# Optimization experiments

Hardware: AMD Instinct MI355X
Metric: run time of the kernel (lower is better)

Reference implementation:

```python
import jax, jax.numpy as jnp
import numpy as np

# Module hyperparameters (init_kwargs)
NH = 254          # nHidden
NSTEP = 32        # MPC horizon
DT = 1.0 / 60.0   # del_t
EPS = 1e-4
PQ = 5.0
QV = 200.0
QA = 1.0
N_STATE = NH + 2  # hidden embedding + [position, velocity]
NBATCH = 256


def setup_inputs() -> dict:
    key = jax.random.key(0)
    k1, k2, k3, k4, k5, k6 = jax.random.split(key, 6)
    x = jax.random.normal(k1, (NBATCH, NH), dtype=jnp.float32)
    gripper_p = jax.random.normal(k2, (NBATCH,), dtype=jnp.float32)
    own_gripper_v = jax.random.normal(k3, (NBATCH,), dtype=jnp.float32)
    other_gripper_v = jax.random.normal(k4, (NBATCH,), dtype=jnp.float32)
    # Learned parameters (as in __init__): Af ~ U[0,1), Lq = tril(U[0,1))
    Af = jax.random.uniform(k5, (NH, 1), dtype=jnp.float32)
    Lq = jnp.tril(jax.random.uniform(k6, (NH, NH), dtype=jnp.float32))
    return {"x": x, "gripper_p": gripper_p, "own_gripper_v": own_gripper_v,
            "other_gripper_v": other_gripper_v, "Af": Af, "Lq": Lq}


def _mpc_forward(x, gripper_p, own_gripper_v, Af, Lq):
    n = N_STATE
    dt = x.dtype
    eye_n = jnp.eye(n, dtype=dt)

    # ---- Q0: [[Lq Lq^T + eps I, 0], [0, diag(0, Qv)]]  (n x n) ----
    Q0_tl = Lq @ Lq.T + EPS * jnp.eye(NH, dtype=dt)
    Q0 = jnp.zeros((n, n), dt).at[:NH, :NH].set(Q0_tl).at[NH + 1, NH + 1].set(QV)
    w = jnp.ones((NSTEP,), dt).at[-1].set(PQ)        # final-step weight Pq
    Q0_stack = w[:, None, None] * Q0                 # [NSTEP, n, n]
    Q_dia = jax.scipy.linalg.block_diag(*Q0_stack)   # [NSTEP*n, NSTEP*n]

    # ---- A0: [[I, 0, Af], [0, 1, dt], [0, 0, 1]] ----
    A0 = jnp.zeros((n, n), dt)
    A0 = A0.at[:NH, :NH].set(jnp.eye(NH, dtype=dt)).at[:NH, NH + 1].set(Af[:, 0])
    A0 = A0.at[NH, NH].set(1.0).at[NH, NH + 1].set(DT).at[NH + 1, NH + 1].set(1.0)

    # ---- powers A0^1..A0^NSTEP via scan (replaces the Python power loop) ----
    def step(carry, _):
        nxt = carry @ A0
        return nxt, nxt
    _, Pk = jax.lax.scan(step, eye_n, None, length=NSTEP)   # Pk[k] = A0^{k+1}
    P = jnp.concatenate([eye_n[None], Pk], axis=0)          # A0^0 .. A0^NSTEP
    T_ = Pk.reshape(NSTEP * n, n)                           # vstack(A0^1..A0^NSTEP)

    # ---- AN_: block lower-triangular Toeplitz, block (i,j) = A0^{i-j} for j<=i ----
    d = jnp.arange(NSTEP)[:, None] - jnp.arange(NSTEP)[None, :]
    blocks = jnp.where((d >= 0)[:, :, None, None],
                       P[jnp.clip(d, 0, NSTEP)], jnp.zeros((), dt))  # [NSTEP,NSTEP,n,n]
    AN_ = blocks.transpose(0, 2, 1, 3).reshape(NSTEP * n, NSTEP * n)

    B0 = jnp.zeros((n, 1), dt).at[NH, 0].set(0.5 * DT * DT).at[NH + 1, 0].set(DT)
    B_dia = jax.scipy.linalg.block_diag(*jnp.broadcast_to(B0, (NSTEP, n, 1)))

    S_ = AN_ @ B_dia                                        # [NSTEP*n, NSTEP]
    QS = Q_dia @ S_                                         # [NSTEP*n, NSTEP]
    Q_final = 2.0 * (QA * jnp.eye(NSTEP, dtype=dt) + S_.T @ QS) \
              + EPS * jnp.eye(NSTEP, dtype=dt)
    p_final = 2.0 * (T_.T @ QS)                             # [n, NSTEP]

    # ---- batch state x0 = [x, gripper_p, own_gripper_v] ----
    x0 = jnp.concatenate([x, gripper_p[:, None], own_gripper_v[:, None]], axis=1)
    p_x0 = x0 @ p_final                                     # [B, NSTEP]

    # QPFunction with G=0, h=0, no equalities -> unconstrained QP:
    # u = argmin 0.5 u^T Q_final u + p_x0^T u = -Q_final^{-1} p_x0
    u = -jnp.linalg.solve(Q_final, p_x0.T).T                # [B, NSTEP]

    # x_predict = S u + T x0 ; output picks position component (index NH) per step
    x_pred = u @ S_.T + x0 @ T_.T                           # [B, NSTEP*n]
    posi = x_pred.reshape(-1, NSTEP, n)[:, :, NH]           # [B, NSTEP]
    return posi


def reference(x, gripper_p, own_gripper_v, other_gripper_v, Af, Lq):
    # other_gripper_v is accepted but unused in the active forward path (as in source)
    return _mpc_forward(x, gripper_p, own_gripper_v, Af, Lq)
```

## Files before the change

kernel.cpp:

```cpp
#include <hip/hip_runtime.h>

#define NH 254
#define NSTEP 32
#define NB 256

constexpr float  FEPS = 1e-4f;
constexpr double DDT  = 1.0 / 60.0;
constexpr double DQV  = 200.0;
constexpr double DPQ  = 5.0;
constexpr double DQA  = 1.0;
constexpr double DEPS = 1e-4;

__global__ __launch_bounds__(256) void k_tg(const float* __restrict__ Lq,
                                            const float* __restrict__ Af,
                                            float* __restrict__ g,
                                            float* __restrict__ coef) {
    __shared__ float t_sh[256];
    __shared__ float af_sh[256];
    const int k    = threadIdx.x;
    const int lane = k & 63;
    const int w    = k >> 6;

    af_sh[k] = (k < NH) ? Af[k] : 0.f;
    __syncthreads();

    float acc = 0.f;
    if (k < NH) {
        #pragma unroll 8
        for (int i = 64 * w; i < NH; ++i)
            acc += Lq[i * NH + k] * af_sh[i];
    }
    t_sh[k] = acc;
    __syncthreads();

    if (blockIdx.x < 32) {
        const int i0 = blockIdx.x * 8;
        for (int rr = 0; rr < 2; ++rr) {
            const int i = i0 + 2 * w + rr;
            if (i >= NH) break;
            float a2 = 0.f;
            #pragma unroll
            for (int c4 = 0; c4 < 4; ++c4) {
                int kk = lane + 64 * c4;
                if (kk <= i) a2 += Lq[i * NH + kk] * t_sh[kk];
            }
            #pragma unroll
            for (int off = 32; off; off >>= 1) a2 += __shfl_xor(a2, off, 64);
            if (lane == 0) g[i] = a2 + FEPS * Af[i];
        }
        return;
    }

    __shared__ double red[4];
    __shared__ double M[32][34];
    __shared__ double ua[32], ub[32];

    double v = 0.0;
    if (k < NH) {
        double td = (double)t_sh[k];
        double ad = (double)af_sh[k];
        v = td * td + DEPS * ad * ad;
    }
    #pragma unroll
    for (int off = 32; off; off >>= 1) v += __shfl_xor(v, off, 64);
    if (lane == 0) red[w] = v;
    __syncthreads();
    const double c = red[0] + red[1] + red[2] + red[3];

    for (int e = k; e < 1024; e += 256) {
        const int j1 = e >> 5, j2 = e & 31;
        const int m = (j1 > j2) ? j1 : j2;
        double s = 0.0;
        for (int kk = m; kk < 32; ++kk) {
            const double wk = (kk == 31) ? DPQ : 1.0;
            s += wk * ((double)(kk - j1) * (double)(kk - j2) * c + DQV);
        }
        M[j1][j2] = 2.0 * DDT * DDT * s + ((j1 == j2) ? (2.0 * DQA + DEPS) : 0.0);
    }
    if (k < 32) {
        const int j = k;
        double sa = 0.0, sb = 0.0;
        for (int kk = j; kk < 32; ++kk) {
            const double wk = (kk == 31) ? DPQ : 1.0;
            sa += wk * (double)(kk - j);
            sb += wk * ((double)(kk + 1) * (double)(kk - j) * c + DQV);
        }
        M[j][32] = 2.0 * DDT * sa;
        M[j][33] = 2.0 * DDT * sb;
    }
    __syncthreads();

    const int r  = k & 31;
    const int cg = k >> 5;
    for (int p = 0; p < 32; ++p) {
        const double f = M[r][p] / M[p][p];
        if (r != p) {
            for (int cc = cg; cc < 34; cc += 8)
                if (cc > p) M[r][cc] -= f * M[p][cc];
        }
        __syncthreads();
    }

    if (k < 32) {
        ua[k] = -M[k][32] / M[k][k];
        ub[k] = -M[k][33] / M[k][k];
    }
    __syncthreads();

    if (k < 32) {
        const int i = k;
        double ca = 0.0, cb = 0.0;
        for (int j = 0; j <= i; ++j) {
            const double wgt = (double)(i - j) + 0.5;
            ca += wgt * ua[j];
            cb += wgt * ub[j];
        }
        ca *= DDT * DDT;
        cb *= DDT * DDT;
        coef[i]      = (float)ca;
        coef[32 + i] = (float)((double)(i + 1) * DDT + cb);
    }
}

__global__ __launch_bounds__(64) void k_out(const float* __restrict__ x,
                                            const float* __restrict__ gp,
                                            const float* __restrict__ gv,
                                            const float* __restrict__ g,
                                            const float* __restrict__ coef,
                                            float* __restrict__ out) {
    const int b = blockIdx.x;
    const int lane = threadIdx.x;
    float acc = 0.f;
    #pragma unroll
    for (int c4 = 0; c4 < 4; ++c4) {
        const int kk = lane + 64 * c4;
        if (kk < NH) acc += x[b * NH + kk] * g[kk];
    }
    #pragma unroll
    for (int off = 32; off; off >>= 1) acc += __shfl_xor(acc, off, 64);
    if (lane < 32) {
        out[b * NSTEP + lane] = gp[b] + gv[b] * coef[32 + lane] + acc * coef[lane];
    }
}

extern "C" void kernel_launch(void* const* d_in, const int* in_sizes, int n_in,
                              void* d_out, int out_size, void* d_ws, size_t ws_size,
                              hipStream_t stream) {
    const float* x  = (const float*)d_in[0];
    const float* gp = (const float*)d_in[1];
    const float* gv = (const float*)d_in[2];
    const float* Af = (const float*)d_in[4];
    const float* Lq = (const float*)d_in[5];
    float* out = (float*)d_out;

    float* ws   = (float*)d_ws;
    float* g    = ws;
    float* coef = ws + 256;

    k_tg<<<33, 256, 0, stream>>>(Lq, Af, g, coef);
    k_out<<<NB, 64, 0, stream>>>(x, gp, gv, g, coef, out);
}
```

Measured before the change: 99.59 us.

## Fuse both kernels into one cooperative kernel with grid-wide syncs

Merges the Lq/Af reduction, the QP coefficient solve and the batched output into a single cooperative launch of 65 blocks. Each of 64 blocks reads four rows of Lq once, writes partial Lq^T·Af sums, and after a grid sync reduces them and reuses its cached rows for the Lq·t product. The block-per-row serial loop of the old first kernel is replaced. This removes a kernel launch and the long sequential column loop, but adds two grid.sync barriers and a 64-way partial reduction through global memory.

```diff
diff --git a/kernel.cpp b/kernel.cpp
--- a/kernel.cpp
+++ b/kernel.cpp
@@ -1,8 +1,12 @@
 #include <hip/hip_runtime.h>
+#include <hip/hip_cooperative_groups.h>
+
+namespace cg = cooperative_groups;
 
 #define NH 254
 #define NSTEP 32
 #define NB 256
+#define NBLK 65
 
 constexpr float  FEPS = 1e-4f;
 constexpr double DDT  = 1.0 / 60.0;
@@ -11,135 +15,162 @@
 constexpr double DQA  = 1.0;
 constexpr double DEPS = 1e-4;
 
-__global__ __launch_bounds__(256) void k_tg(const float* __restrict__ Lq,
-                                            const float* __restrict__ Af,
-                                            float* __restrict__ g,
-                                            float* __restrict__ coef) {
-    __shared__ float t_sh[256];
-    __shared__ float af_sh[256];
+__global__ __launch_bounds__(256) void k_all(const float* __restrict__ Lq,
+                                             const float* __restrict__ Af,
+                                             const float* __restrict__ x,
+                                             const float* __restrict__ gp,
+                                             const float* __restrict__ gv,
+                                             float* __restrict__ ws,
+                                             float* __restrict__ out) {
+    float* partial = ws;
+    float* g       = ws + 64 * 256;
+    float* coef    = g + 256;
+
+    __shared__ float  lq_sh[4][256];
+    __shared__ float  sh[256];
+    __shared__ double red[4];
+    __shared__ double M[32][34];
+    __shared__ double ua[32], ub[32];
+
+    const int bid  = blockIdx.x;
     const int k    = threadIdx.x;
     const int lane = k & 63;
     const int w    = k >> 6;
 
-    af_sh[k] = (k < NH) ? Af[k] : 0.f;
-    __syncthreads();
+    cg::grid_group grid = cg::this_grid();
 
-    float acc = 0.f;
-    if (k < NH) {
-        #pragma unroll 8
-        for (int i = 64 * w; i < NH; ++i)
-            acc += Lq[i * NH + k] * af_sh[i];
+    float xr[4] = {0.f, 0.f, 0.f, 0.f};
+    float gpv = 0.f, gvv = 0.f;
+
+    if (bid < 64) {
+        float lqv[4];
+        #pragma unroll
+        for (int j = 0; j < 4; ++j) {
+            const int i = 4 * bid + j;
+            lqv[j] = (i < NH && k < NH) ? Lq[i * NH + k] : 0.f;
+        }
+        const int r = 4 * bid + w;
+        #pragma unroll
+        for (int c4 = 0; c4 < 4; ++c4) {
+            const int kk = lane + 64 * c4;
+            xr[c4] = (kk < NH) ? x[r * NH + kk] : 0.f;
+        }
+        gpv = gp[r];
+        gvv = gv[r];
+
+        float acc = 0.f;
+        #pragma unroll
+        for (int j = 0; j < 4; ++j) {
+            const int i = 4 * bid + j;
+            const float afv = (i < NH) ? Af[i] : 0.f;
+            lq_sh[j][k] = lqv[j];
+            acc += lqv[j] * afv;
+        }
+        partial[bid * 256 + k] = acc;
     }
-    t_sh[k] = acc;
-    __syncthreads();
+    grid.sync();
 
-    if (blockIdx.x < 32) {
-        const int i0 = blockIdx.x * 8;
-        for (int rr = 0; rr < 2; ++rr) {
-            const int i = i0 + 2 * w + rr;
-            if (i >= NH) break;
-            float a2 = 0.f;
-            #pragma unroll
-            for (int c4 = 0; c4 < 4; ++c4) {
-                int kk = lane + 64 * c4;
-                if (kk <= i) a2 += Lq[i * NH + kk] * t_sh[kk];
-            }
-            #pragma unroll
-            for (int off = 32; off; off >>= 1) a2 += __shfl_xor(a2, off, 64);
-            if (lane == 0) g[i] = a2 + FEPS * Af[i];
-        }
-        return;
-    }
-
-    __shared__ double red[4];
-    __shared__ double M[32][34];
-    __shared__ double ua[32], ub[32];
-
-    double v = 0.0;
-    if (k < NH) {
-        double td = (double)t_sh[k];
-        double ad = (double)af_sh[k];
-        v = td * td + DEPS * ad * ad;
-    }
-    #pragma unroll
-    for (int off = 32; off; off >>= 1) v += __shfl_xor(v, off, 64);
-    if (lane == 0) red[w] = v;
-    __syncthreads();
-    const double c = red[0] + red[1] + red[2] + red[3];
-
-    for (int e = k; e < 1024; e += 256) {
-        const int j1 = e >> 5, j2 = e & 31;
-        const int m = (j1 > j2) ? j1 : j2;
-        double s = 0.0;
-        for (int kk = m; kk < 32; ++kk) {
-            const double wk = (kk == 31) ? DPQ : 1.0;
-            s += wk * ((double)(kk - j1) * (double)(kk - j2) * c + DQV);
-        }
-        M[j1][j2] = 2.0 * DDT * DDT * s + ((j1 == j2) ? (2.0 * DQA + DEPS) : 0.0);
-    }
-    if (k < 32) {
-        const int j = k;
-        double sa = 0.0, sb = 0.0;
-        for (int kk = j; kk < 32; ++kk) {
-            const double wk = (kk == 31) ? DPQ : 1.0;
-            sa += wk * (double)(kk - j);
-            sb += wk * ((double)(kk + 1) * (double)(kk - j) * c + DQV);
-        }
-        M[j][32] = 2.0 * DDT * sa;
-        M[j][33] = 2.0 * DDT * sb;
+    {
+        float tk = 0.f;
+        #pragma unroll 16
+        for (int b = 0; b < 64; ++b) tk += partial[b * 256 + k];
+        sh[k] = tk;
     }
     __syncthreads();
 
-    const int r  = k & 31;
-    const int cg = k >> 5;
-    for (int p = 0; p < 32; ++p) {
-        const double f = M[r][p] / M[p][p];
-        if (r != p) {
-            for (int cc = cg; cc < 34; cc += 8)
-                if (cc > p) M[r][cc] -= f * M[p][cc];
+    if (bid < 64) {
+        const int i = 4 * bid + w;
+        float a2 = 0.f;
+        #pragma unroll
+        for (int c4 = 0; c4 < 4; ++c4) {
+            const int kk = lane + 64 * c4;
+            a2 += lq_sh[w][kk] * sh[kk];
+        }
+        #pragma unroll
+        for (int off = 32; off; off >>= 1) a2 += __shfl_xor(a2, off, 64);
+        if (lane == 0 && i < NH) g[i] = a2 + FEPS * Af[i];
+    } else {
+        double v = 0.0;
+        if (k < NH) {
+            const double td = (double)sh[k];
+            const double ad = (double)Af[k];
+            v = td * td + DEPS * ad * ad;
+        }
+        #pragma unroll
+        for (int off = 32; off; off >>= 1) v += __shfl_xor(v, off, 64);
+        if (lane == 0) red[w] = v;
+        __syncthreads();
+        const double c = red[0] + red[1] + red[2] + red[3];
+
+        for (int e = k; e < 1024; e += 256) {
+            const int j1 = e >> 5, j2 = e & 31;
+            const int m = (j1 > j2) ? j1 : j2;
+            double s = 0.0;
+            for (int kk = m; kk < 32; ++kk) {
+                const double wk = (kk == 31) ? DPQ : 1.0;
+                s += wk * ((double)(kk - j1) * (double)(kk - j2) * c + DQV);
+            }
+            M[j1][j2] = 2.0 * DDT * DDT * s + ((j1 == j2) ? (2.0 * DQA + DEPS) : 0.0);
+        }
+        if (k < 32) {
+            const int j = k;
+            double sa = 0.0, sb = 0.0;
+            for (int kk = j; kk < 32; ++kk) {
+                const double wk = (kk == 31) ? DPQ : 1.0;
+                sa += wk * (double)(kk - j);
+                sb += wk * ((double)(kk + 1) * (double)(kk - j) * c + DQV);
+            }
+            M[j][32] = 2.0 * DDT * sa;
+            M[j][33] = 2.0 * DDT * sb;
         }
         __syncthreads();
+
+        const int r   = k & 31;
+        const int cg8 = k >> 5;
+        for (int p = 0; p < 32; ++p) {
+            const double f = M[r][p] / M[p][p];
+            if (r != p) {
+                for (int cc = cg8; cc < 34; cc += 8)
+                    if (cc > p) M[r][cc] -= f * M[p][cc];
+            }
+            __syncthreads();
+        }
+
+        if (k < 32) {
+            ua[k] = -M[k][32] / M[k][k];
+            ub[k] = -M[k][33] / M[k][k];
+        }
+        __syncthreads();
+
+        if (k < 32) {
+            const int i = k;
+            double ca = 0.0, cb = 0.0;
+            for (int j = 0; j <= i; ++j) {
+                const double wgt = (double)(i - j) + 0.5;
+                ca += wgt * ua[j];
+                cb += wgt * ub[j];
+            }
+            ca *= DDT * DDT;
+            cb *= DDT * DDT;
+            coef[i]      = (float)ca;
+            coef[32 + i] = (float)((double)(i + 1) * DDT + cb);
+        }
     }
+    __threadfence();
+    grid.sync();
 
-    if (k < 32) {
-        ua[k] = -M[k][32] / M[k][k];
-        ub[k] = -M[k][33] / M[k][k];
-    }
-    __syncthreads();
-
-    if (k < 32) {
-        const int i = k;
-        double ca = 0.0, cb = 0.0;
-        for (int j = 0; j <= i; ++j) {
-            const double wgt = (double)(i - j) + 0.5;
-            ca += wgt * ua[j];
-            cb += wgt * ub[j];
-        }
-        ca *= DDT * DDT;
-        cb *= DDT * DDT;
-        coef[i]      = (float)ca;
-        coef[32 + i] = (float)((double)(i + 1) * DDT + cb);
-    }
-}
-
-__global__ __launch_bounds__(64) void k_out(const float* __restrict__ x,
-                                            const float* __restrict__ gp,
-                                            const float* __restrict__ gv,
-                                            const float* __restrict__ g,
-                                            const float* __restrict__ coef,
-                                            float* __restrict__ out) {
-    const int b = blockIdx.x;
-    const int lane = threadIdx.x;
-    float acc = 0.f;
-    #pragma unroll
-    for (int c4 = 0; c4 < 4; ++c4) {
-        const int kk = lane + 64 * c4;
-        if (kk < NH) acc += x[b * NH + kk] * g[kk];
-    }
-    #pragma unroll
-    for (int off = 32; off; off >>= 1) acc += __shfl_xor(acc, off, 64);
-    if (lane < 32) {
-        out[b * NSTEP + lane] = gp[b] + gv[b] * coef[32 + lane] + acc * coef[lane];
+    if (bid < 64) {
+        sh[k] = (k < NH) ? g[k] : 0.f;
+        __syncthreads();
+        float s = 0.f;
+        #pragma unroll
+        for (int c4 = 0; c4 < 4; ++c4)
+            s += xr[c4] * sh[lane + 64 * c4];
+        #pragma unroll
+        for (int off = 32; off; off >>= 1) s += __shfl_xor(s, off, 64);
+        const int r = 4 * bid + w;
+        if (lane < 32)
+            out[r * NSTEP + lane] = gpv + gvv * coef[32 + lane] + s * coef[lane];
     }
 }
 
@@ -152,11 +183,10 @@
     const float* Af = (const float*)d_in[4];
     const float* Lq = (const float*)d_in[5];
     float* out = (float*)d_out;
+    float* ws  = (float*)d_ws;
 
-    float* ws   = (float*)d_ws;
-    float* g    = ws;
-    float* coef = ws + 256;
-
-    k_tg<<<33, 256, 0, stream>>>(Lq, Af, g, coef);
-    k_out<<<NB, 64, 0, stream>>>(x, gp, gv, g, coef, out);
+    void* args[] = {(void*)&Lq, (void*)&Af, (void*)&x, (void*)&gp, (void*)&gv,
+                    (void*)&ws, (void*)&out};
+    hipLaunchCooperativeKernel((const void*)k_all, dim3(NBLK), dim3(256),
+                               args, 0, stream);
 }
```

Result: slower. 125.1 us (+25.6%).

## Fuse both kernels into a single 1024-thread monolithic block

Applied to the files above, without the earlier changes.

Replaces the two-kernel pipeline (33-block setup kernel plus 256-block output kernel) with one 1024-thread single-block kernel. Lq·Af is split across four thread quarters, g = Lq t is kept in shared memory, and the 32x32 Gauss-Jordan solve plus the batch outputs are all computed in the same block. This removes one launch and the global round trip for g and coef, and drops the redundant per-block recomputation of t. In exchange, all Lq and x traffic now goes through a single CU, with far less memory parallelism.

```diff
diff --git a/kernel.cpp b/kernel.cpp
--- a/kernel.cpp
+++ b/kernel.cpp
@@ -11,64 +11,98 @@
 constexpr double DQA  = 1.0;
 constexpr double DEPS = 1e-4;
 
-__global__ __launch_bounds__(256) void k_tg(const float* __restrict__ Lq,
-                                            const float* __restrict__ Af,
-                                            float* __restrict__ g,
-                                            float* __restrict__ coef) {
-    __shared__ float t_sh[256];
-    __shared__ float af_sh[256];
-    const int k    = threadIdx.x;
-    const int lane = k & 63;
-    const int w    = k >> 6;
-
-    af_sh[k] = (k < NH) ? Af[k] : 0.f;
-    __syncthreads();
-
-    float acc = 0.f;
-    if (k < NH) {
-        #pragma unroll 8
-        for (int i = 64 * w; i < NH; ++i)
-            acc += Lq[i * NH + k] * af_sh[i];
-    }
-    t_sh[k] = acc;
-    __syncthreads();
-
-    if (blockIdx.x < 32) {
-        const int i0 = blockIdx.x * 8;
-        for (int rr = 0; rr < 2; ++rr) {
-            const int i = i0 + 2 * w + rr;
-            if (i >= NH) break;
-            float a2 = 0.f;
-            #pragma unroll
-            for (int c4 = 0; c4 < 4; ++c4) {
-                int kk = lane + 64 * c4;
-                if (kk <= i) a2 += Lq[i * NH + kk] * t_sh[kk];
-            }
-            #pragma unroll
-            for (int off = 32; off; off >>= 1) a2 += __shfl_xor(a2, off, 64);
-            if (lane == 0) g[i] = a2 + FEPS * Af[i];
-        }
-        return;
-    }
-
+__global__ __launch_bounds__(1024) void k_mono(const float* __restrict__ Lq,
+                                               const float* __restrict__ Af,
+                                               const float* __restrict__ x,
+                                               const float* __restrict__ gp,
+                                               const float* __restrict__ gv,
+                                               float* __restrict__ out) {
+    __shared__ float  af_sh[256];
+    __shared__ float  tpart[4][256];
+    __shared__ float  t_sh[256];
+    __shared__ float  g_sh[256];
     __shared__ double red[4];
     __shared__ double M[32][34];
     __shared__ double ua[32], ub[32];
+    __shared__ float  cA[32], cB[32];
 
-    double v = 0.0;
-    if (k < NH) {
-        double td = (double)t_sh[k];
-        double ad = (double)af_sh[k];
-        v = td * td + DEPS * ad * ad;
+    const int tid  = threadIdx.x;
+    const int k8   = tid & 255;
+    const int q    = tid >> 8;
+    const int lane = tid & 63;
+    const int wv   = tid >> 6;
+
+    if (q == 0) af_sh[k8] = (k8 < NH) ? Af[k8] : 0.f;
+    if (tid == 0) { g_sh[254] = 0.f; g_sh[255] = 0.f; }
+    __syncthreads();
+
+    {
+        float acc = 0.f;
+        const int ibase = q * 64;
+        if (k8 < NH && k8 < ibase + 64) {
+            const int iend = (ibase + 64 < NH) ? ibase + 64 : NH;
+            for (int i0 = ibase; i0 < iend; i0 += 8) {
+                float v[8];
+                #pragma unroll
+                for (int j = 0; j < 8; ++j)
+                    v[j] = (i0 + j < iend) ? Lq[(i0 + j) * NH + k8] : 0.f;
+                #pragma unroll
+                for (int j = 0; j < 8; ++j)
+                    acc += v[j] * af_sh[i0 + j];
+            }
+        }
+        tpart[q][k8] = acc;
     }
-    #pragma unroll
-    for (int off = 32; off; off >>= 1) v += __shfl_xor(v, off, 64);
-    if (lane == 0) red[w] = v;
+    __syncthreads();
+    if (tid < 256)
+        t_sh[tid] = tpart[0][tid] + tpart[1][tid] + tpart[2][tid] + tpart[3][tid];
+    __syncthreads();
+
+    for (int r = 0; r < 16; r += 2) {
+        const int i1 = wv + 16 * r;
+        const int i2 = i1 + 16;
+        float lv1[4], lv2[4];
+        #pragma unroll
+        for (int c = 0; c < 4; ++c) {
+            const int kk = lane + 64 * c;
+            lv1[c] = (kk <= i1) ? Lq[i1 * NH + kk] : 0.f;
+            lv2[c] = (i2 < NH && kk <= i2) ? Lq[i2 * NH + kk] : 0.f;
+        }
+        float a1 = 0.f, a2 = 0.f;
+        #pragma unroll
+        for (int c = 0; c < 4; ++c) {
+            const int kk = lane + 64 * c;
+            a1 += lv1[c] * t_sh[kk];
+            a2 += lv2[c] * t_sh[kk];
+        }
+        #pragma unroll
+        for (int off = 32; off; off >>= 1) {
+            a1 += __shfl_xor(a1, off, 64);
+            a2 += __shfl_xor(a2, off, 64);
+        }
+        if (lane == 0) {
+            g_sh[i1] = a1 + FEPS * af_sh[i1];
+            if (i2 < NH) g_sh[i2] = a2 + FEPS * af_sh[i2];
+        }
+    }
+    __syncthreads();
+
+    {
+        double dv = 0.0;
+        if (tid < NH) {
+            const double td = (double)t_sh[tid];
+            const double ad = (double)af_sh[tid];
+            dv = td * td + DEPS * ad * ad;
+        }
+        #pragma unroll
+        for (int off = 32; off; off >>= 1) dv += __shfl_xor(dv, off, 64);
+        if (wv < 4 && lane == 0) red[wv] = dv;
+    }
     __syncthreads();
     const double c = red[0] + red[1] + red[2] + red[3];
 
-    for (int e = k; e < 1024; e += 256) {
-        const int j1 = e >> 5, j2 = e & 31;
+    {
+        const int j1 = tid >> 5, j2 = tid & 31;
         const int m = (j1 > j2) ? j1 : j2;
         double s = 0.0;
         for (int kk = m; kk < 32; ++kk) {
@@ -77,8 +111,8 @@
         }
         M[j1][j2] = 2.0 * DDT * DDT * s + ((j1 == j2) ? (2.0 * DQA + DEPS) : 0.0);
     }
-    if (k < 32) {
-        const int j = k;
+    if (tid < 32) {
+        const int j = tid;
         double sa = 0.0, sb = 0.0;
         for (int kk = j; kk < 32; ++kk) {
             const double wk = (kk == 31) ? DPQ : 1.0;
@@ -90,56 +124,63 @@
     }
     __syncthreads();
 
-    const int r  = k & 31;
-    const int cg = k >> 5;
-    for (int p = 0; p < 32; ++p) {
-        const double f = M[r][p] / M[p][p];
-        if (r != p) {
-            for (int cc = cg; cc < 34; cc += 8)
-                if (cc > p) M[r][cc] -= f * M[p][cc];
+    {
+        const int r  = tid & 31;
+        const int cg = tid >> 5;
+        for (int p = 0; p < 32; ++p) {
+            const double f = M[r][p] / M[p][p];
+            if (r != p) {
+                if (cg > p) M[r][cg] -= f * M[p][cg];
+                const int c2 = cg + 32;
+                if (c2 < 34) M[r][c2] -= f * M[p][c2];
+            }
+            __syncthreads();
         }
-        __syncthreads();
     }
-
-    if (k < 32) {
-        ua[k] = -M[k][32] / M[k][k];
-        ub[k] = -M[k][33] / M[k][k];
+    if (tid < 32) {
+        ua[tid] = -M[tid][32] / M[tid][tid];
+        ub[tid] = -M[tid][33] / M[tid][tid];
     }
     __syncthreads();
-
-    if (k < 32) {
-        const int i = k;
+    if (tid < 32) {
+        const int i = tid;
         double ca = 0.0, cb = 0.0;
         for (int j = 0; j <= i; ++j) {
             const double wgt = (double)(i - j) + 0.5;
             ca += wgt * ua[j];
             cb += wgt * ub[j];
         }
-        ca *= DDT * DDT;
-        cb *= DDT * DDT;
-        coef[i]      = (float)ca;
-        coef[32 + i] = (float)((double)(i + 1) * DDT + cb);
+        cA[i] = (float)(ca * DDT * DDT);
+        cB[i] = (float)((double)(i + 1) * DDT + cb * DDT * DDT);
     }
-}
+    __syncthreads();
 
-__global__ __launch_bounds__(64) void k_out(const float* __restrict__ x,
-                                            const float* __restrict__ gp,
-                                            const float* __restrict__ gv,
-                                            const float* __restrict__ g,
-                                            const float* __restrict__ coef,
-                                            float* __restrict__ out) {
-    const int b = blockIdx.x;
-    const int lane = threadIdx.x;
-    float acc = 0.f;
-    #pragma unroll
-    for (int c4 = 0; c4 < 4; ++c4) {
-        const int kk = lane + 64 * c4;
-        if (kk < NH) acc += x[b * NH + kk] * g[kk];
-    }
-    #pragma unroll
-    for (int off = 32; off; off >>= 1) acc += __shfl_xor(acc, off, 64);
-    if (lane < 32) {
-        out[b * NSTEP + lane] = gp[b] + gv[b] * coef[32 + lane] + acc * coef[lane];
+    for (int r = 0; r < 16; r += 2) {
+        const int b1 = wv + 16 * r;
+        const int b2 = b1 + 16;
+        float xa[4], xb[4];
+        #pragma unroll
+        for (int cidx = 0; cidx < 4; ++cidx) {
+            const int kk = lane + 64 * cidx;
+            xa[cidx] = (kk < NH) ? x[b1 * NH + kk] : 0.f;
+            xb[cidx] = (kk < NH) ? x[b2 * NH + kk] : 0.f;
+        }
+        float s1 = 0.f, s2 = 0.f;
+        #pragma unroll
+        for (int cidx = 0; cidx < 4; ++cidx) {
+            const int kk = lane + 64 * cidx;
+            s1 += xa[cidx] * g_sh[kk];
+            s2 += xb[cidx] * g_sh[kk];
+        }
+        #pragma unroll
+        for (int off = 32; off; off >>= 1) {
+            s1 += __shfl_xor(s1, off, 64);
+            s2 += __shfl_xor(s2, off, 64);
+        }
+        if (lane < 32) {
+            out[b1 * NSTEP + lane] = gp[b1] + gv[b1] * cB[lane] + s1 * cA[lane];
+            out[b2 * NSTEP + lane] = gp[b2] + gv[b2] * cB[lane] + s2 * cA[lane];
+        }
     }
 }
 
@@ -153,10 +194,5 @@
     const float* Lq = (const float*)d_in[5];
     float* out = (float*)d_out;
 
-    float* ws   = (float*)d_ws;
-    float* g    = ws;
-    float* coef = ws + 256;
-
-    k_tg<<<33, 256, 0, stream>>>(Lq, Af, g, coef);
-    k_out<<<NB, 64, 0, stream>>>(x, gp, gv, g, coef, out);
+    k_mono<<<1, 1024, 0, stream>>>(Lq, Af, x, gp, gv, out);
 }
```

Measured after the change: 93.16 us. 1.07x faster.
